# Kernel optimization log

Hardware: AMD Instinct MI355X
Metric: run time of the kernel (lower is better)

Reference implementation:

```python
import jax, jax.numpy as jnp
import numpy as np

N = 50000        # nodes
E = 1600000      # edges (avg degree 32)
H = 128          # hidden_channels == num_filters
G = 50           # num_gaussians
L = 5            # num_interactions
CUTOFF = 4.5
VOCAB = 100
LOG2 = float(np.log(2.0))


def setup_inputs() -> dict:
    key = jax.random.key(0)
    ks = jax.random.split(key, 12)
    s = 1.0 / np.sqrt(H)
    sg = 1.0 / np.sqrt(G)
    atomic_numbers = jax.random.randint(ks[0], (N,), 0, VOCAB, dtype=jnp.int32)
    edge_index = jax.random.randint(ks[1], (2, E), 0, N, dtype=jnp.int32)
    edge_attr = jax.random.uniform(ks[2], (E,), dtype=jnp.float32)
    emb = jax.random.normal(ks[3], (VOCAB, H), dtype=jnp.float32) * 0.1
    emb = emb.at[0].set(0.0)  # padding_idx=0
    Wi = jax.random.normal(ks[4], (L, H, H), dtype=jnp.float32) * s
    bi = jnp.zeros((L, H), dtype=jnp.float32)
    Wn = jax.random.normal(ks[5], (L, G, H), dtype=jnp.float32) * sg
    bn = jnp.zeros((L, H), dtype=jnp.float32)
    Wo = jax.random.normal(ks[6], (L, H, H), dtype=jnp.float32) * s
    bo = jnp.zeros((L, H), dtype=jnp.float32)
    Wl = jax.random.normal(ks[7], (L, H, H), dtype=jnp.float32) * s
    bl = jnp.zeros((L, H), dtype=jnp.float32)
    return {"atomic_numbers": atomic_numbers, "edge_index": edge_index,
            "edge_attr": edge_attr, "emb": emb,
            "Wi": Wi, "bi": bi, "Wn": Wn, "bn": bn,
            "Wo": Wo, "bo": bo, "Wl": Wl, "bl": bl}


def _gaussian_smearing(dist):
    offsets = jnp.linspace(0.0, CUTOFF, G, dtype=jnp.float32)
    coeff = -0.5 / (offsets[1] - offsets[0]) ** 2
    return jnp.exp(coeff * (dist[:, None] - offsets[None, :]) ** 2)  # [E, G]


def reference(atomic_numbers, edge_index, edge_attr, emb,
              Wi, bi, Wn, bn, Wo, bo, Wl, bl):
    src, dst = edge_index[0], edge_index[1]
    x = emb[atomic_numbers]                      # [N, H]
    gauss = _gaussian_smearing(edge_attr)        # [E, G]
    C = 0.5 * (jnp.cos(edge_attr * jnp.pi / CUTOFF) + 1.0)  # cosine cutoff [E]
    for l in range(L):
        W = (gauss @ Wn[l] + bn[l]) * C[:, None]   # edge filters [E, H]
        h = x @ Wi[l] + bi[l]                       # [N, H]
        msg = h[src] * W                            # gather + filter [E, H]
        agg = jax.ops.segment_sum(msg, dst, num_segments=N)  # scatter-add [N, H]
        h = agg @ Wo[l] + bo[l]
        h = jax.nn.softplus(h) - LOG2               # shifted softplus
        h = h @ Wl[l] + bl[l]
        x = x + h                                   # residual
    return x
```

## Files before the change

### kernel.cpp

```cpp
#include <hip/hip_runtime.h>
#include <hip/hip_bf16.h>

#define HDIM 128
#define NG 50
#define NL 5
#define TBN 4096
#define CAP 96
#define CAPB 9000
#define CHUNK 8192

static constexpr float CUTOFF_F = 4.5f;
static constexpr float PI_F = 3.14159265358979323846f;
static constexpr float LN2_F = 0.6931471805599453f;

typedef __attribute__((ext_vector_type(8))) short bf16x8;
typedef __attribute__((ext_vector_type(4))) float f32x4;

__device__ __forceinline__ unsigned f2bfbits(float f) {
    unsigned b = __float_as_uint(f);
    return (b + 0x7FFFu + ((b >> 16) & 1u)) >> 16;
}
__device__ __forceinline__ float bflo(unsigned u) { return __uint_as_float(u << 16); }
__device__ __forceinline__ float bfhi(unsigned u) { return __uint_as_float(u & 0xFFFF0000u); }

__device__ __forceinline__ float softplus_shifted(float v) {
    return fmaxf(v, 0.0f) + __logf(1.0f + __expf(-fabsf(v))) - LN2_F;
}

__device__ __forceinline__ bf16x8 ldB(const unsigned short* __restrict__ W,
                                      int nn, int kc, int l4) {
    return *reinterpret_cast<const bf16x8*>(W + nn * HDIM + kc * 32 + l4 * 8);
}

__global__ __launch_bounds__(256) void embed_kernel(
    const int* __restrict__ an, const float* __restrict__ emb,
    float* __restrict__ x, int n)
{
    int idx = blockIdx.x * 256 + threadIdx.x;
    int total = n * (HDIM / 4);
    if (idx >= total) return;
    int i = idx >> 5;
    int j = idx & 31;
    int a = an[i];
    reinterpret_cast<float4*>(x)[(size_t)i * 32 + j] =
        reinterpret_cast<const float4*>(emb)[(size_t)a * 32 + j];
}

__global__ __launch_bounds__(256) void prep_weights(
    const float* __restrict__ Wi, const float* __restrict__ Wo,
    const float* __restrict__ Wl, unsigned short* __restrict__ Wt)
{
    int b = blockIdx.x;
    int l = b / 3, m = b % 3;
    const float* src = (m == 0 ? Wi : (m == 1 ? Wo : Wl)) + (size_t)l * HDIM * HDIM;
    unsigned short* dst = Wt + (size_t)b * HDIM * HDIM;
    for (int idx = threadIdx.x; idx < HDIM * HDIM; idx += 256) {
        int k = idx >> 7, n = idx & 127;
        dst[n * HDIM + k] = (unsigned short)f2bfbits(src[k * HDIM + n]);
    }
}

__global__ __launch_bounds__(128) void build_tables_all(
    const float* __restrict__ Wn, const float* __restrict__ bn,
    unsigned short* __restrict__ T)
{
    __shared__ float gs[NG];
    int p = blockIdx.x;
    int l = blockIdx.y;
    int j = threadIdx.x;
    const float* Wnl = Wn + (size_t)l * NG * HDIM;
    float d = (float)p * (1.0f / (float)TBN);
    if (j < NG) {
        const float delta = CUTOFF_F / (float)(NG - 1);
        const float coeff = -0.5f / (delta * delta);
        float t = d - (float)j * delta;
        gs[j] = expf(coeff * t * t);
    }
    __syncthreads();
    float acc = bn[(size_t)l * HDIM + j];
    #pragma unroll 10
    for (int g = 0; g < NG; ++g) acc = fmaf(gs[g], Wnl[g * HDIM + j], acc);
    acc *= 0.5f * (cosf(d * (PI_F / CUTOFF_F)) + 1.0f);
    T[((size_t)l * (TBN + 1) + p) * HDIM + j] = (unsigned short)f2bfbits(acc);
}

__global__ __launch_bounds__(512) void bucket_pass(
    const int* __restrict__ src, const int* __restrict__ dstp,
    const float* __restrict__ attr, int* __restrict__ gbase,
    uint2* __restrict__ buf, int E, int nbuck)
{
    __shared__ int hist[256], cur[256], base_l[256];
    const int tid = threadIdx.x;
    if (tid < 256) { hist[tid] = 0; cur[tid] = 0; }
    __syncthreads();
    const int e0 = blockIdx.x * CHUNK;
    int myd[CHUNK / 512];
    #pragma unroll
    for (int k = 0; k < CHUNK / 512; ++k) {
        int e = e0 + k * 512 + tid;
        myd[k] = (e < E) ? dstp[e] : -1;
        if (myd[k] >= 0) atomicAdd(&hist[myd[k] >> 8], 1);
    }
    __syncthreads();
    if (tid < nbuck)
        base_l[tid] = hist[tid] ? atomicAdd(&gbase[tid], hist[tid]) : 0;
    __syncthreads();
    #pragma unroll
    for (int k = 0; k < CHUNK / 512; ++k) {
        int d = myd[k];
        if (d < 0) continue;
        int e = e0 + k * 512 + tid;
        int b = d >> 8;
        int rank = atomicAdd(&cur[b], 1);
        int pos = base_l[b] + rank;
        unsigned ii = (unsigned)(int)fminf(attr[e] * (float)TBN + 0.5f, (float)TBN);
        if (pos < CAPB)
            buf[(size_t)b * CAPB + pos] = make_uint2((ii << 16) | (unsigned)src[e], (unsigned)d);
    }
}

__global__ __launch_bounds__(512) void bin_pass(
    const int* __restrict__ gtot, const uint2* __restrict__ buf,
    unsigned* __restrict__ sp, int* __restrict__ cnt, int N)
{
    __shared__ int cl[256];
    const int b = blockIdx.x;
    const int tid = threadIdx.x;
    if (tid < 256) cl[tid] = 0;
    __syncthreads();
    int total = gtot[b];
    if (total > CAPB) total = CAPB;
    const uint2* rb = buf + (size_t)b * CAPB;
    for (int i = tid; i < total; i += 512) {
        uint2 r = rb[i];
        int node = (int)r.y;
        int slot = atomicAdd(&cl[node & 255], 1);
        if (slot < CAP) sp[(size_t)node * CAP + slot] = r.x;
    }
    __syncthreads();
    if (tid < 256) {
        int node = b * 256 + tid;
        if (node < N) cnt[node] = min(cl[tid], CAP);
    }
}

__global__ __launch_bounds__(256) void mfma_gemm0(
    const float* __restrict__ A, const unsigned short* __restrict__ Wt,
    const float* __restrict__ bias, unsigned short* __restrict__ outp, int M)
{
    __shared__ unsigned short Ls[64 * HDIM];
    const int tid = threadIdx.x;
    const int row0 = blockIdx.x * 64;

    #pragma unroll
    for (int it = 0; it < 8; ++it) {
        int idx = it * 256 + tid;
        int r = idx >> 5;
        int k2 = (idx & 31) * 8;
        int row = row0 + r;
        float4 v = make_float4(0.f, 0.f, 0.f, 0.f);
        if (row < M) v = reinterpret_cast<const float4*>(A)[(size_t)row * 32 + (idx & 31)];
        uint2 u;
        u.x = f2bfbits(v.x) | (f2bfbits(v.y) << 16);
        u.y = f2bfbits(v.z) | (f2bfbits(v.w) << 16);
        *reinterpret_cast<uint2*>(reinterpret_cast<char*>(Ls) +
            r * 256 + (k2 ^ ((r & 7) << 4))) = u;
    }
    __syncthreads();

    const int wid = tid >> 6, lane = tid & 63;
    const int wr = wid >> 1, wc = wid & 1;
    const int l15 = lane & 15, l4 = lane >> 4;

    f32x4 acc[2][4] = {};
    bf16x8 afrag[2][4];
    #pragma unroll
    for (int m = 0; m < 2; ++m)
        #pragma unroll
        for (int kc = 0; kc < 4; ++kc) {
            int r = wr * 32 + m * 16 + l15;
            int k2 = (kc * 32 + l4 * 8) * 2;
            afrag[m][kc] = *reinterpret_cast<const bf16x8*>(
                reinterpret_cast<const char*>(Ls) + r * 256 + (k2 ^ ((r & 7) << 4)));
        }
    __syncthreads();
    #pragma unroll
    for (int n = 0; n < 4; ++n)
        #pragma unroll
        for (int kc = 0; kc < 4; ++kc) {
            bf16x8 bfrag = ldB(Wt, wc * 64 + n * 16 + l15, kc, l4);
            #pragma unroll
            for (int m = 0; m < 2; ++m)
                acc[m][n] = __builtin_amdgcn_mfma_f32_16x16x32_bf16(
                    afrag[m][kc], bfrag, acc[m][n], 0, 0, 0);
        }
    #pragma unroll
    for (int n = 0; n < 4; ++n) {
        int col = wc * 64 + n * 16 + l15;
        float bv = bias[col];
        #pragma unroll
        for (int m = 0; m < 2; ++m)
            #pragma unroll
            for (int r = 0; r < 4; ++r) {
                int rl = wr * 32 + m * 16 + l4 * 4 + r;
                Ls[rl * HDIM + col] = (unsigned short)f2bfbits(acc[m][n][r] + bv);
            }
    }
    __syncthreads();
    #pragma unroll
    for (int it = 0; it < 4; ++it) {
        int e = it * 256 + tid;
        int row = row0 + (e >> 4);
        if (row < M)
            reinterpret_cast<uint4*>(outp)[(size_t)row0 * 16 + e] =
                reinterpret_cast<const uint4*>(Ls)[e];
    }
}

template<int LAST>
__global__ __launch_bounds__(512) void gemm_fused(
    const unsigned short* __restrict__ aggb, const unsigned short* __restrict__ Wot,
    const float* __restrict__ bo, const unsigned short* __restrict__ Wlt,
    const float* __restrict__ bl, float* __restrict__ x,
    const unsigned short* __restrict__ Wit, const float* __restrict__ bi_,
    unsigned short* __restrict__ hb, int M)
{
    __shared__ unsigned short Ls[64 * HDIM];
    const int tid = threadIdx.x;
    const int row0 = blockIdx.x * 64;
    const int wid = tid >> 6, lane = tid & 63;
    const int wr = wid >> 1, wc = wid & 1;
    const int l15 = lane & 15, l4 = lane >> 4;

    const unsigned short* ag =
        aggb + (size_t)(row0 + wr * 16 + l15) * HDIM + l4 * 8;
    f32x4 acc1[4] = {};
    bf16x8 af[4];
    #pragma unroll
    for (int kc = 0; kc < 4; ++kc)
        af[kc] = *reinterpret_cast<const bf16x8*>(ag + kc * 32);
    #pragma unroll
    for (int n = 0; n < 4; ++n)
        #pragma unroll
        for (int kc = 0; kc < 4; ++kc) {
            bf16x8 bfrag = ldB(Wot, wc * 64 + n * 16 + l15, kc, l4);
            acc1[n] = __builtin_amdgcn_mfma_f32_16x16x32_bf16(af[kc], bfrag, acc1[n], 0, 0, 0);
        }

    #pragma unroll
    for (int n = 0; n < 4; ++n) {
        int col = wc * 64 + n * 16 + l15;
        float bv = bo[col];
        #pragma unroll
        for (int r = 0; r < 4; ++r) {
            int rl = wr * 16 + l4 * 4 + r;
            float v = softplus_shifted(acc1[n][r] + bv);
            *reinterpret_cast<unsigned short*>(reinterpret_cast<char*>(Ls) +
                rl * 256 + ((2 * col) ^ ((rl & 7) << 4))) = (unsigned short)f2bfbits(v);
        }
    }
    __syncthreads();

    {
        int r = wr * 16 + l15;
        #pragma unroll
        for (int kc = 0; kc < 4; ++kc) {
            int k2 = (kc * 32 + l4 * 8) * 2;
            af[kc] = *reinterpret_cast<const bf16x8*>(
                reinterpret_cast<const char*>(Ls) + r * 256 + (k2 ^ ((r & 7) << 4)));
        }
    }
    __syncthreads();
    f32x4 acc2[4] = {};
    #pragma unroll
    for (int n = 0; n < 4; ++n)
        #pragma unroll
        for (int kc = 0; kc < 4; ++kc) {
            bf16x8 bfrag = ldB(Wlt, wc * 64 + n * 16 + l15, kc, l4);
            acc2[n] = __builtin_amdgcn_mfma_f32_16x16x32_bf16(af[kc], bfrag, acc2[n], 0, 0, 0);
        }

    #pragma unroll
    for (int n = 0; n < 4; ++n) {
        int col = wc * 64 + n * 16 + l15;
        float bv = bl[col];
        #pragma unroll
        for (int r = 0; r < 4; ++r) {
            int rl = wr * 16 + l4 * 4 + r;
            int row = row0 + rl;
            float v = acc2[n][r] + bv;
            if (row < M) {
                float* o = x + (size_t)row * HDIM + col;
                v += *o;
                *o = v;
            }
            if (!LAST)
                *reinterpret_cast<unsigned short*>(reinterpret_cast<char*>(Ls) +
                    rl * 256 + ((2 * col) ^ ((rl & 7) << 4))) = (unsigned short)f2bfbits(v);
        }
    }
    if (LAST) return;
    __syncthreads();

    {
        int r = wr * 16 + l15;
        #pragma unroll
        for (int kc = 0; kc < 4; ++kc) {
            int k2 = (kc * 32 + l4 * 8) * 2;
            af[kc] = *reinterpret_cast<const bf16x8*>(
                reinterpret_cast<const char*>(Ls) + r * 256 + (k2 ^ ((r & 7) << 4)));
        }
    }
    __syncthreads();
    f32x4 acc3[4] = {};
    #pragma unroll
    for (int n = 0; n < 4; ++n)
        #pragma unroll
        for (int kc = 0; kc < 4; ++kc) {
            bf16x8 bfrag = ldB(Wit, wc * 64 + n * 16 + l15, kc, l4);
            acc3[n] = __builtin_amdgcn_mfma_f32_16x16x32_bf16(af[kc], bfrag, acc3[n], 0, 0, 0);
        }
    #pragma unroll
    for (int n = 0; n < 4; ++n) {
        int col = wc * 64 + n * 16 + l15;
        float bv = bi_[col];
        #pragma unroll
        for (int r = 0; r < 4; ++r) {
            int rl = wr * 16 + l4 * 4 + r;
            Ls[rl * HDIM + col] = (unsigned short)f2bfbits(acc3[n][r] + bv);
        }
    }
    __syncthreads();
    #pragma unroll
    for (int it = 0; it < 2; ++it) {
        int e = it * 512 + tid;
        int row = row0 + (e >> 4);
        if (row < M)
            reinterpret_cast<uint4*>(hb)[(size_t)row0 * 16 + e] =
                reinterpret_cast<const uint4*>(Ls)[e];
    }
}

#define ACC8(hv, tv) \
    a0 = fmaf(bflo(hv.x), bflo(tv.x), a0); a1 = fmaf(bfhi(hv.x), bfhi(tv.x), a1); \
    a2 = fmaf(bflo(hv.y), bflo(tv.y), a2); a3 = fmaf(bfhi(hv.y), bfhi(tv.y), a3); \
    a4 = fmaf(bflo(hv.z), bflo(tv.z), a4); a5 = fmaf(bfhi(hv.z), bfhi(tv.z), a5); \
    a6 = fmaf(bflo(hv.w), bflo(tv.w), a6); a7 = fmaf(bfhi(hv.w), bfhi(tv.w), a7);

__global__ __launch_bounds__(256) void agg_kernel(
    const int* __restrict__ cnt, const unsigned* __restrict__ sp,
    const unsigned short* __restrict__ T,
    const unsigned* __restrict__ hb,
    unsigned* __restrict__ aggb, int n)
{
    const int tid = threadIdx.x;
    const int lane = tid & 63;
    const int g = lane >> 4;
    const int c16 = lane & 15;
    const int node = (blockIdx.x * 256 + tid) >> 6;
    if (node >= n) return;

    const int deg = cnt[node];
    const unsigned* recs = sp + (size_t)node * CAP;
    const uint4* T4 = reinterpret_cast<const uint4*>(T);
    const uint4* h4 = reinterpret_cast<const uint4*>(hb);

    float a0 = 0.f, a1 = 0.f, a2 = 0.f, a3 = 0.f;
    float a4 = 0.f, a5 = 0.f, a6 = 0.f, a7 = 0.f;

    int i = 0;
    for (; i + 8 <= deg; i += 8) {
        unsigned ra = recs[i + g];
        unsigned rb = recs[i + 4 + g];
        uint4 ta = T4[(size_t)(ra >> 16) * 16 + c16];
        uint4 ha = h4[(size_t)(ra & 0xFFFFu) * 16 + c16];
        uint4 tb = T4[(size_t)(rb >> 16) * 16 + c16];
        uint4 hbv = h4[(size_t)(rb & 0xFFFFu) * 16 + c16];
        ACC8(ha, ta)
        ACC8(hbv, tb)
    }
    for (int base = i; base < deg; base += 4) {
        int e = base + g;
        unsigned r = (e < deg) ? recs[e] : 0u;
        uint4 tv = T4[(size_t)(r >> 16) * 16 + c16];
        uint4 hv = make_uint4(0u, 0u, 0u, 0u);
        if (e < deg) hv = h4[(size_t)(r & 0xFFFFu) * 16 + c16];
        ACC8(hv, tv)
    }

    a0 += __shfl_xor(a0, 16); a1 += __shfl_xor(a1, 16);
    a2 += __shfl_xor(a2, 16); a3 += __shfl_xor(a3, 16);
    a4 += __shfl_xor(a4, 16); a5 += __shfl_xor(a5, 16);
    a6 += __shfl_xor(a6, 16); a7 += __shfl_xor(a7, 16);
    a0 += __shfl_xor(a0, 32); a1 += __shfl_xor(a1, 32);
    a2 += __shfl_xor(a2, 32); a3 += __shfl_xor(a3, 32);
    a4 += __shfl_xor(a4, 32); a5 += __shfl_xor(a5, 32);
    a6 += __shfl_xor(a6, 32); a7 += __shfl_xor(a7, 32);

    if (g == 0) {
        uint4 o;
        o.x = f2bfbits(a0) | (f2bfbits(a1) << 16);
        o.y = f2bfbits(a2) | (f2bfbits(a3) << 16);
        o.z = f2bfbits(a4) | (f2bfbits(a5) << 16);
        o.w = f2bfbits(a6) | (f2bfbits(a7) << 16);
        reinterpret_cast<uint4*>(aggb)[(size_t)node * 16 + c16] = o;
    }
}

extern "C" void kernel_launch(void* const* d_in, const int* in_sizes, int n_in,
                              void* d_out, int out_size, void* d_ws, size_t ws_size,
                              hipStream_t stream)
{
    const int*   an   = (const int*)d_in[0];
    const int*   ei   = (const int*)d_in[1];
    const float* attr = (const float*)d_in[2];
    const float* emb  = (const float*)d_in[3];
    const float* Wi   = (const float*)d_in[4];
    const float* bi   = (const float*)d_in[5];
    const float* Wn   = (const float*)d_in[6];
    const float* bn   = (const float*)d_in[7];
    const float* Wo   = (const float*)d_in[8];
    const float* bo   = (const float*)d_in[9];
    const float* Wl   = (const float*)d_in[10];
    const float* bl   = (const float*)d_in[11];

    const int N = in_sizes[0];
    const int E = in_sizes[2];
    const int* srcp = ei;
    const int* dstp = ei + E;
    const int nbuck = (N + 255) >> 8;

    float* x = (float*)d_out;

    char* w = (char*)d_ws;
    unsigned*       aggb = (unsigned*)w;      w += (size_t)N * HDIM * 2;
    unsigned*       hb   = (unsigned*)w;      w += (size_t)N * HDIM * 2;
    unsigned short* T    = (unsigned short*)w; w += (size_t)NL * (TBN + 1) * HDIM * 2;
    unsigned short* Wt   = (unsigned short*)w; w += (size_t)NL * 3 * HDIM * HDIM * 2;
    int*            cnt  = (int*)w;           w += (size_t)N * 4;
    int*            gbase= (int*)w;           w += 256 * 4;
    unsigned*       sp   = (unsigned*)w;      w += (size_t)N * CAP * 4;
    uint2*          buf  = (uint2*)aggb;

    prep_weights<<<NL * 3, 256, 0, stream>>>(Wi, Wo, Wl, Wt);
    embed_kernel<<<(N * 32 + 255) / 256, 256, 0, stream>>>(an, emb, x, N);
    build_tables_all<<<dim3(TBN + 1, NL), 128, 0, stream>>>(Wn, bn, T);

    hipMemsetAsync(gbase, 0, 256 * sizeof(int), stream);
    bucket_pass<<<(E + CHUNK - 1) / CHUNK, 512, 0, stream>>>(
        srcp, dstp, attr, gbase, buf, E, nbuck);
    bin_pass<<<nbuck, 512, 0, stream>>>(gbase, buf, sp, cnt, N);

    const int gemm_grid = (N + 63) / 64;
    const int agg_grid  = (N + 3) / 4;

    mfma_gemm0<<<gemm_grid, 256, 0, stream>>>(x, Wt, bi, (unsigned short*)hb, N);

    for (int l = 0; l < NL; ++l) {
        agg_kernel<<<agg_grid, 256, 0, stream>>>(
            cnt, sp, T + (size_t)l * (TBN + 1) * HDIM, hb, aggb, N);
        if (l < NL - 1) {
            gemm_fused<0><<<gemm_grid, 512, 0, stream>>>(
                (unsigned short*)aggb, Wt + (size_t)(l * 3 + 1) * HDIM * HDIM, bo + (size_t)l * HDIM,
                Wt + (size_t)(l * 3 + 2) * HDIM * HDIM, bl + (size_t)l * HDIM, x,
                Wt + (size_t)((l + 1) * 3 + 0) * HDIM * HDIM, bi + (size_t)(l + 1) * HDIM,
                (unsigned short*)hb, N);
        } else {
            gemm_fused<1><<<gemm_grid, 512, 0, stream>>>(
                (unsigned short*)aggb, Wt + (size_t)(l * 3 + 1) * HDIM * HDIM, bo + (size_t)l * HDIM,
                Wt + (size_t)(l * 3 + 2) * HDIM * HDIM, bl + (size_t)l * HDIM, x,
                Wt, bi, (unsigned short*)hb, N);
        }
    }
}
```

Measured before the change: 757.7 us.

## Restructure fused node GEMM so each wave owns 16 full rows without block barriers

The fused Wo/softplus/Wl/residual/Wi kernel now gives each of four waves 16 complete rows across all 128 columns. MFMA operands are swapped so each lane holds four consecutive columns, which allows float4 bias, residual and x accesses. Each wave uses its own swizzled LDS tile, so all __syncthreads are removed and the block shrinks from 512 to 256 threads. In exchange each wave does twice the MFMAs and weight loads per GEMM and holds eight accumulators, which raises register pressure.

```diff
diff --git a/kernel.cpp b/kernel.cpp
--- a/kernel.cpp
+++ b/kernel.cpp
@@ -25,11 +25,6 @@
 
 __device__ __forceinline__ float softplus_shifted(float v) {
     return fmaxf(v, 0.0f) + __logf(1.0f + __expf(-fabsf(v))) - LN2_F;
-}
-
-__device__ __forceinline__ bf16x8 ldB(const unsigned short* __restrict__ W,
-                                      int nn, int kc, int l4) {
-    return *reinterpret_cast<const bf16x8*>(W + nn * HDIM + kc * 32 + l4 * 8);
 }
 
 __global__ __launch_bounds__(256) void embed_kernel(
@@ -142,6 +137,11 @@
         int node = b * 256 + tid;
         if (node < N) cnt[node] = min(cl[tid], CAP);
     }
+}
+
+__device__ __forceinline__ bf16x8 ldB(const unsigned short* __restrict__ W,
+                                      int nn, int kc, int l4) {
+    return *reinterpret_cast<const bf16x8*>(W + nn * HDIM + kc * 32 + l4 * 8);
 }
 
 __global__ __launch_bounds__(256) void mfma_gemm0(
@@ -218,126 +218,123 @@
 }
 
 template<int LAST>
-__global__ __launch_bounds__(512) void gemm_fused(
+__global__ __launch_bounds__(256) void gemm_fused(
     const unsigned short* __restrict__ aggb, const unsigned short* __restrict__ Wot,
     const float* __restrict__ bo, const unsigned short* __restrict__ Wlt,
     const float* __restrict__ bl, float* __restrict__ x,
     const unsigned short* __restrict__ Wit, const float* __restrict__ bi_,
     unsigned short* __restrict__ hb, int M)
 {
-    __shared__ unsigned short Ls[64 * HDIM];
+    __shared__ unsigned short Ls[4][16 * HDIM];
     const int tid = threadIdx.x;
+    const int w = tid >> 6, lane = tid & 63;
+    const int l15 = lane & 15, l4 = lane >> 4;
     const int row0 = blockIdx.x * 64;
-    const int wid = tid >> 6, lane = tid & 63;
-    const int wr = wid >> 1, wc = wid & 1;
-    const int l15 = lane & 15, l4 = lane >> 4;
-
-    const unsigned short* ag =
-        aggb + (size_t)(row0 + wr * 16 + l15) * HDIM + l4 * 8;
-    f32x4 acc1[4] = {};
-    bf16x8 af[4];
-    #pragma unroll
-    for (int kc = 0; kc < 4; ++kc)
-        af[kc] = *reinterpret_cast<const bf16x8*>(ag + kc * 32);
-    #pragma unroll
-    for (int n = 0; n < 4; ++n)
-        #pragma unroll
-        for (int kc = 0; kc < 4; ++kc) {
-            bf16x8 bfrag = ldB(Wot, wc * 64 + n * 16 + l15, kc, l4);
-            acc1[n] = __builtin_amdgcn_mfma_f32_16x16x32_bf16(af[kc], bfrag, acc1[n], 0, 0, 0);
-        }
-
-    #pragma unroll
-    for (int n = 0; n < 4; ++n) {
-        int col = wc * 64 + n * 16 + l15;
-        float bv = bo[col];
-        #pragma unroll
-        for (int r = 0; r < 4; ++r) {
-            int rl = wr * 16 + l4 * 4 + r;
-            float v = softplus_shifted(acc1[n][r] + bv);
-            *reinterpret_cast<unsigned short*>(reinterpret_cast<char*>(Ls) +
-                rl * 256 + ((2 * col) ^ ((rl & 7) << 4))) = (unsigned short)f2bfbits(v);
-        }
-    }
-    __syncthreads();
-
-    {
-        int r = wr * 16 + l15;
-        #pragma unroll
-        for (int kc = 0; kc < 4; ++kc) {
-            int k2 = (kc * 32 + l4 * 8) * 2;
-            af[kc] = *reinterpret_cast<const bf16x8*>(
-                reinterpret_cast<const char*>(Ls) + r * 256 + (k2 ^ ((r & 7) << 4)));
-        }
-    }
-    __syncthreads();
-    f32x4 acc2[4] = {};
-    #pragma unroll
-    for (int n = 0; n < 4; ++n)
-        #pragma unroll
-        for (int kc = 0; kc < 4; ++kc) {
-            bf16x8 bfrag = ldB(Wlt, wc * 64 + n * 16 + l15, kc, l4);
-            acc2[n] = __builtin_amdgcn_mfma_f32_16x16x32_bf16(af[kc], bfrag, acc2[n], 0, 0, 0);
-        }
-
-    #pragma unroll
-    for (int n = 0; n < 4; ++n) {
-        int col = wc * 64 + n * 16 + l15;
-        float bv = bl[col];
-        #pragma unroll
-        for (int r = 0; r < 4; ++r) {
-            int rl = wr * 16 + l4 * 4 + r;
-            int row = row0 + rl;
-            float v = acc2[n][r] + bv;
-            if (row < M) {
-                float* o = x + (size_t)row * HDIM + col;
-                v += *o;
-                *o = v;
-            }
-            if (!LAST)
-                *reinterpret_cast<unsigned short*>(reinterpret_cast<char*>(Ls) +
-                    rl * 256 + ((2 * col) ^ ((rl & 7) << 4))) = (unsigned short)f2bfbits(v);
+    const int gm = row0 + w * 16 + l15;
+    const int gmr = min(gm, M - 1);
+    char* Lb = reinterpret_cast<char*>(Ls[w]);
+    const int swz = (l15 & 7) << 4;
+
+    const unsigned short* agp = aggb + (size_t)gmr * HDIM + l4 * 8;
+    bf16x8 bq[4];
+    #pragma unroll
+    for (int kc = 0; kc < 4; ++kc)
+        bq[kc] = *reinterpret_cast<const bf16x8*>(agp + kc * 32);
+
+    f32x4 acc[8];
+    #pragma unroll
+    for (int j = 0; j < 8; ++j) acc[j] = f32x4{0.f, 0.f, 0.f, 0.f};
+    #pragma unroll
+    for (int kc = 0; kc < 4; ++kc)
+        #pragma unroll
+        for (int j = 0; j < 8; ++j) {
+            bf16x8 wf = *reinterpret_cast<const bf16x8*>(
+                Wot + (size_t)(j * 16 + l15) * HDIM + kc * 32 + l4 * 8);
+            acc[j] = __builtin_amdgcn_mfma_f32_16x16x32_bf16(wf, bq[kc], acc[j], 0, 0, 0);
+        }
+
+    const float* xp = x + (size_t)gmr * HDIM + l4 * 4;
+    float4 xv[8];
+    #pragma unroll
+    for (int j = 0; j < 8; ++j)
+        xv[j] = *reinterpret_cast<const float4*>(xp + j * 16);
+
+    #pragma unroll
+    for (int j = 0; j < 8; ++j) {
+        float4 b4 = *reinterpret_cast<const float4*>(bo + j * 16 + l4 * 4);
+        uint2 u;
+        u.x = f2bfbits(softplus_shifted(acc[j][0] + b4.x)) |
+              (f2bfbits(softplus_shifted(acc[j][1] + b4.y)) << 16);
+        u.y = f2bfbits(softplus_shifted(acc[j][2] + b4.z)) |
+              (f2bfbits(softplus_shifted(acc[j][3] + b4.w)) << 16);
+        *reinterpret_cast<uint2*>(Lb + l15 * 256 + ((32 * j + 8 * l4) ^ swz)) = u;
+    }
+
+    bf16x8 tq[4];
+    #pragma unroll
+    for (int kc = 0; kc < 4; ++kc)
+        tq[kc] = *reinterpret_cast<const bf16x8*>(Lb + l15 * 256 + ((64 * kc + 16 * l4) ^ swz));
+    #pragma unroll
+    for (int j = 0; j < 8; ++j) acc[j] = f32x4{0.f, 0.f, 0.f, 0.f};
+    #pragma unroll
+    for (int kc = 0; kc < 4; ++kc)
+        #pragma unroll
+        for (int j = 0; j < 8; ++j) {
+            bf16x8 wf = *reinterpret_cast<const bf16x8*>(
+                Wlt + (size_t)(j * 16 + l15) * HDIM + kc * 32 + l4 * 8);
+            acc[j] = __builtin_amdgcn_mfma_f32_16x16x32_bf16(wf, tq[kc], acc[j], 0, 0, 0);
+        }
+
+    #pragma unroll
+    for (int j = 0; j < 8; ++j) {
+        float4 b4 = *reinterpret_cast<const float4*>(bl + j * 16 + l4 * 4);
+        float4 v;
+        v.x = acc[j][0] + b4.x + xv[j].x;
+        v.y = acc[j][1] + b4.y + xv[j].y;
+        v.z = acc[j][2] + b4.z + xv[j].z;
+        v.w = acc[j][3] + b4.w + xv[j].w;
+        if (gm < M)
+            *reinterpret_cast<float4*>(const_cast<float*>(xp) + j * 16) = v;
+        if (!LAST) {
+            uint2 u;
+            u.x = f2bfbits(v.x) | (f2bfbits(v.y) << 16);
+            u.y = f2bfbits(v.z) | (f2bfbits(v.w) << 16);
+            *reinterpret_cast<uint2*>(Lb + l15 * 256 + ((32 * j + 8 * l4) ^ swz)) = u;
         }
     }
     if (LAST) return;
-    __syncthreads();
-
-    {
-        int r = wr * 16 + l15;
-        #pragma unroll
-        for (int kc = 0; kc < 4; ++kc) {
-            int k2 = (kc * 32 + l4 * 8) * 2;
-            af[kc] = *reinterpret_cast<const bf16x8*>(
-                reinterpret_cast<const char*>(Ls) + r * 256 + (k2 ^ ((r & 7) << 4)));
-        }
-    }
-    __syncthreads();
-    f32x4 acc3[4] = {};
-    #pragma unroll
-    for (int n = 0; n < 4; ++n)
-        #pragma unroll
-        for (int kc = 0; kc < 4; ++kc) {
-            bf16x8 bfrag = ldB(Wit, wc * 64 + n * 16 + l15, kc, l4);
-            acc3[n] = __builtin_amdgcn_mfma_f32_16x16x32_bf16(af[kc], bfrag, acc3[n], 0, 0, 0);
-        }
-    #pragma unroll
-    for (int n = 0; n < 4; ++n) {
-        int col = wc * 64 + n * 16 + l15;
-        float bv = bi_[col];
-        #pragma unroll
-        for (int r = 0; r < 4; ++r) {
-            int rl = wr * 16 + l4 * 4 + r;
-            Ls[rl * HDIM + col] = (unsigned short)f2bfbits(acc3[n][r] + bv);
-        }
-    }
-    __syncthreads();
-    #pragma unroll
-    for (int it = 0; it < 2; ++it) {
-        int e = it * 512 + tid;
-        int row = row0 + (e >> 4);
-        if (row < M)
-            reinterpret_cast<uint4*>(hb)[(size_t)row0 * 16 + e] =
-                reinterpret_cast<const uint4*>(Ls)[e];
+
+    #pragma unroll
+    for (int kc = 0; kc < 4; ++kc)
+        tq[kc] = *reinterpret_cast<const bf16x8*>(Lb + l15 * 256 + ((64 * kc + 16 * l4) ^ swz));
+    #pragma unroll
+    for (int j = 0; j < 8; ++j) acc[j] = f32x4{0.f, 0.f, 0.f, 0.f};
+    #pragma unroll
+    for (int kc = 0; kc < 4; ++kc)
+        #pragma unroll
+        for (int j = 0; j < 8; ++j) {
+            bf16x8 wf = *reinterpret_cast<const bf16x8*>(
+                Wit + (size_t)(j * 16 + l15) * HDIM + kc * 32 + l4 * 8);
+            acc[j] = __builtin_amdgcn_mfma_f32_16x16x32_bf16(wf, tq[kc], acc[j], 0, 0, 0);
+        }
+    #pragma unroll
+    for (int j = 0; j < 8; ++j) {
+        float4 b4 = *reinterpret_cast<const float4*>(bi_ + j * 16 + l4 * 4);
+        uint2 u;
+        u.x = f2bfbits(acc[j][0] + b4.x) | (f2bfbits(acc[j][1] + b4.y) << 16);
+        u.y = f2bfbits(acc[j][2] + b4.z) | (f2bfbits(acc[j][3] + b4.w) << 16);
+        *reinterpret_cast<uint2*>(Lb + l15 * 256 + ((32 * j + 8 * l4) ^ swz)) = u;
+    }
+    #pragma unroll
+    for (int it = 0; it < 4; ++it) {
+        int e = it * 64 + lane;
+        int rr = e >> 4;
+        int row = row0 + w * 16 + rr;
+        if (row < M) {
+            uint4 v = *reinterpret_cast<const uint4*>(
+                Lb + rr * 256 + ((16 * (e & 15)) ^ ((rr & 7) << 4)));
+            reinterpret_cast<uint4*>(hb)[(size_t)row * 16 + (e & 15)] = v;
+        }
     }
 }
 
@@ -460,13 +457,13 @@
         agg_kernel<<<agg_grid, 256, 0, stream>>>(
             cnt, sp, T + (size_t)l * (TBN + 1) * HDIM, hb, aggb, N);
         if (l < NL - 1) {
-            gemm_fused<0><<<gemm_grid, 512, 0, stream>>>(
+            gemm_fused<0><<<gemm_grid, 256, 0, stream>>>(
                 (unsigned short*)aggb, Wt + (size_t)(l * 3 + 1) * HDIM * HDIM, bo + (size_t)l * HDIM,
                 Wt + (size_t)(l * 3 + 2) * HDIM * HDIM, bl + (size_t)l * HDIM, x,
                 Wt + (size_t)((l + 1) * 3 + 0) * HDIM * HDIM, bi + (size_t)(l + 1) * HDIM,
                 (unsigned short*)hb, N);
         } else {
-            gemm_fused<1><<<gemm_grid, 512, 0, stream>>>(
+            gemm_fused<1><<<gemm_grid, 256, 0, stream>>>(
                 (unsigned short*)aggb, Wt + (size_t)(l * 3 + 1) * HDIM * HDIM, bo + (size_t)l * HDIM,
                 Wt + (size_t)(l * 3 + 2) * HDIM * HDIM, bl + (size_t)l * HDIM, x,
                 Wt, bi, (unsigned short*)hb, N);
```

Result: faster. 738.6 us (-2.5%).
